# Performance work log

Hardware: AMD Instinct MI355X
Metric: run time of the kernel (lower is better)

Reference implementation:

```python
import jax, jax.numpy as jnp
import numpy as np


def _conv1d(x, w, b, pad):
    # x: (BN, Cin, L), w: (Cout, Cin, K) torch OIH layout
    y = jax.lax.conv_general_dilated(x, w, window_strides=(1,), padding=[(pad, pad)],
                                     dimension_numbers=('NCH', 'OIH', 'NCH'))
    return y + b[None, :, None]


def _mask_conv(m, k):
    # all-ones kernel conv then >=1 threshold (matches constant-init mask convs, no_grad)
    w = jnp.ones((1, 1, k), m.dtype)
    y = jax.lax.conv_general_dilated(m, w, window_strides=(1,), padding=[((k - 1) // 2, (k - 1) // 2)],
                                     dimension_numbers=('NCH', 'OIH', 'NCH'))
    return (y >= 1.0).astype(m.dtype)


def _branch(x, m, w1, b1, w2, b2, k):
    pad = (k - 1) // 2
    o = jax.nn.relu(_conv1d(x, w1, b1, pad))
    m = jax.lax.stop_gradient(_mask_conv(m, k))
    o = o * m
    o = jax.nn.relu(_conv1d(o, w2, b2, pad))
    m = jax.lax.stop_gradient(_mask_conv(m, k))
    return o * m


def _forward(all_xanes, all_xanes_mask, all_elem_info, all_elem_mask,
             w_b1c1, b_b1c1, w_b1c2, b_b1c2,
             w_b2c1, b_b2c1, w_b2c2, b_b2c2,
             w_b3c1, b_b3c1, w_b3c2, b_b3c2,
             w_xfc, b_xfc,
             w_float, b_float, atom_emb, type_emb,
             w_fuse, b_fuse,
             in_w, in_b, out_w, out_b,
             w_fc1, b_fc1, w_fc2, b_fc2):
    B, N, L = all_xanes.shape
    E, H = 64, 4
    dh = E // H
    # ---- MultiScaleXANESExtractor ----
    x = all_xanes.reshape(B * N, 1, L)
    m3 = jnp.broadcast_to(all_xanes_mask.reshape(B * N, 1, 1).astype(jnp.float32), (B * N, 1, L))
    o1 = _branch(x, m3, w_b1c1, b_b1c1, w_b1c2, b_b1c2, 3)
    o2 = _branch(x, m3, w_b2c1, b_b2c1, w_b2c2, b_b2c2, 5)
    o3 = _branch(x, m3, w_b3c1, b_b3c1, w_b3c2, b_b3c2, 7)
    cat = jnp.concatenate([o1, o2, o3], axis=1)  # (BN, 384, L)
    pooled = cat.reshape(B * N, 384, 10, L // 10).mean(-1).reshape(B * N, -1)  # AdaptiveAvgPool1d(10)
    xfeat = (pooled @ w_xfc.T + b_xfc).reshape(B, N, -1)  # (B, N, 32)
    valid = (m3.sum(axis=(1, 2)) > 0).astype(jnp.float32).reshape(B, N, 1)
    xfeat = xfeat * valid
    # ---- ElementsFeatureProcessor (vectorized gathers) ----
    maskf = all_elem_mask.astype(jnp.float32)
    masked = all_elem_info * maskf[..., None]
    ff = jax.nn.relu(masked[..., :5] @ w_float.T + b_float)  # (B, N, 16)
    an = masked[..., 5].astype(jnp.int32)
    et = masked[..., 6].astype(jnp.int32)
    valid_e = (maskf >= 0.5)
    inrange = (an >= 1) & (an <= 94)
    take = (valid_e & inrange).astype(jnp.float32)[..., None]
    ez = atom_emb[jnp.clip(an, 0, 94)] * take            # (B, N, 8)
    ety = type_emb[jnp.clip(et, 0, 5)] * take            # (B, N, 4)
    ff = ff * valid_e.astype(jnp.float32)[..., None]
    efeat = jnp.concatenate([ff, ez, ety], axis=-1) * maskf[..., None]  # (B, N, 28)
    # ---- FuseElementAndXANES ----
    fused = jnp.concatenate([xfeat, efeat], axis=-1) @ w_fuse.T + b_fuse
    fused = fused * maskf[..., None]  # (B, N, 64)
    # ---- AttentionAggregator (nn.MultiheadAttention, batch_first) ----
    qkv = fused @ in_w.T + in_b
    q, k, v = jnp.split(qkv, 3, axis=-1)
    q = q.reshape(B, N, H, dh)
    k = k.reshape(B, N, H, dh)
    v = v.reshape(B, N, H, dh)
    scores = jnp.einsum('bqhd,bkhd->bhqk', q, k) / jnp.sqrt(jnp.float32(dh))
    keymask = (maskf >= 0.5)
    scores = jnp.where(keymask[:, None, None, :], scores, jnp.float32(-1e30))
    attn = jax.nn.softmax(scores, axis=-1)
    ao = jnp.einsum('bhqk,bkhd->bqhd', attn, v).reshape(B, N, E)
    ao = ao @ out_w.T + out_b
    ao = ao * maskf[..., None]
    pooled2 = ao.sum(axis=1) / (maskf.sum(axis=1, keepdims=True) + 1e-8)
    h = jax.nn.relu(pooled2 @ w_fc1.T + b_fc1)
    return h @ w_fc2.T + b_fc2  # (B, num_classes)


def setup_inputs():
    key = jax.random.key(0)
    ks = jax.random.split(key, 40)
    B, N, L = 32, 16, 200
    all_xanes = jax.random.normal(ks[0], (B, N, L), jnp.float32)
    all_xanes_mask = jax.random.randint(ks[1], (B, N), 0, 2).astype(jnp.float32)
    ef = jax.random.normal(ks[2], (B, N, 7), jnp.float32)
    an = jax.random.randint(ks[3], (B, N), 1, 95).astype(jnp.float32)
    et = jax.random.randint(ks[4], (B, N), 0, 6).astype(jnp.float32)
    all_elem_info = ef.at[..., 5].set(an).at[..., 6].set(et)
    all_elem_mask = jax.random.randint(ks[5], (B, N), 0, 2).astype(jnp.float32)
    all_elem_mask = all_elem_mask.at[:, 0].set(1.0)  # avoid fully-padded rows (NaN softmax)

    def p(k, shape):
        return jax.random.normal(k, shape, jnp.float32) * 0.05

    inp = dict(all_xanes=all_xanes, all_xanes_mask=all_xanes_mask,
               all_elem_info=all_elem_info, all_elem_mask=all_elem_mask,
               w_b1c1=p(ks[6], (64, 1, 3)), b_b1c1=p(ks[7], (64,)),
               w_b1c2=p(ks[8], (128, 64, 3)), b_b1c2=p(ks[9], (128,)),
               w_b2c1=p(ks[10], (64, 1, 5)), b_b2c1=p(ks[11], (64,)),
               w_b2c2=p(ks[12], (128, 64, 5)), b_b2c2=p(ks[13], (128,)),
               w_b3c1=p(ks[14], (64, 1, 7)), b_b3c1=p(ks[15], (64,)),
               w_b3c2=p(ks[16], (128, 64, 7)), b_b3c2=p(ks[17], (128,)),
               w_xfc=p(ks[18], (32, 3840)), b_xfc=p(ks[19], (32,)),
               w_float=p(ks[20], (16, 5)), b_float=p(ks[21], (16,)),
               atom_emb=p(ks[22], (95, 8)), type_emb=p(ks[23], (6, 4)),
               w_fuse=p(ks[24], (64, 60)), b_fuse=p(ks[25], (64,)),
               in_w=p(ks[26], (192, 64)), in_b=p(ks[27], (192,)),
               out_w=p(ks[28], (64, 64)), out_b=p(ks[29], (64,)),
               w_fc1=p(ks[30], (64, 64)), b_fc1=p(ks[31], (64,)),
               w_fc2=p(ks[32], (1, 64)), b_fc2=p(ks[33], (1,)))
    return inp


def reference(all_xanes, all_xanes_mask, all_elem_info, all_elem_mask,
              w_b1c1, b_b1c1, w_b1c2, b_b1c2,
              w_b2c1, b_b2c1, w_b2c2, b_b2c2,
              w_b3c1, b_b3c1, w_b3c2, b_b3c2,
              w_xfc, b_xfc, w_float, b_float, atom_emb, type_emb,
              w_fuse, b_fuse, in_w, in_b, out_w, out_b,
              w_fc1, b_fc1, w_fc2, b_fc2):
    return _forward(all_xanes, all_xanes_mask, all_elem_info, all_elem_mask,
                    w_b1c1, b_b1c1, w_b1c2, b_b1c2,
                    w_b2c1, b_b2c1, w_b2c2, b_b2c2,
                    w_b3c1, b_b3c1, w_b3c2, b_b3c2,
                    w_xfc, b_xfc, w_float, b_float, atom_emb, type_emb,
                    w_fuse, b_fuse, in_w, in_b, out_w, out_b,
                    w_fc1, b_fc1, w_fc2, b_fc2)
```

## Files before the change

### kernel.cpp

```cpp
#include <hip/hip_runtime.h>
#include <math.h>

typedef float f32x4 __attribute__((ext_vector_type(4)));
typedef short short8 __attribute__((ext_vector_type(8)));

__device__ __forceinline__ short bf16r(float f) {
    union { float f; unsigned u; } x; x.f = f;
    unsigned u = x.u + 0x7fffu + ((x.u >> 16) & 1u);
    return (short)(u >> 16);
}

template<int K>
__device__ __forceinline__ void pack_branch(const float* __restrict__ w2,
                                            short* __restrict__ wpack, int u) {
    int lane = u & 63;
    int kb   = (u >> 6) & 1;
    int rem  = u >> 7;
    int j = rem % K, c = rem / K;
    int co  = c * 16 + (lane & 15);
    int cib = kb * 32 + 8 * ((lane >> 4) & 3);
    short8 v;
    #pragma unroll
    for (int i = 0; i < 8; ++i)
        v[i] = bf16r(w2[(co * 64 + (cib + i)) * K + j]);
    *reinterpret_cast<short8*>(wpack + (size_t)u * 8) = v;
}

__global__ __launch_bounds__(256) void pack_kernel(
    const float* __restrict__ w23, const float* __restrict__ w25,
    const float* __restrict__ w27,
    short* __restrict__ wp3, short* __restrict__ wp5, short* __restrict__ wp7)
{
    int tid = blockIdx.x * 256 + threadIdx.x;
    const int n3 = 8 * 3 * 2 * 64;
    const int n5 = 8 * 5 * 2 * 64;
    const int n7 = 8 * 7 * 2 * 64;
    if (tid < n3)                pack_branch<3>(w23, wp3, tid);
    else if (tid < n3 + n5)      pack_branch<5>(w25, wp5, tid - n3);
    else if (tid < n3 + n5 + n7) pack_branch<7>(w27, wp7, tid - n3 - n5);
}

template<int K, int LT0, int NLT>
__device__ __forceinline__ void mfma2c_pass(
    const short* t1s, const short* wpB0, const short* wpB1,
    int lane, f32x4* accA, f32x4* accB)
{
    constexpr int PAD = (K - 1) / 2;
    const int lane15 = lane & 15;
    const int g      = (lane >> 4) & 3;
    #pragma unroll
    for (int m = 0; m < 2 * K; ++m) {
        const int j = m >> 1, kb = m & 1;
        const short8 B0 = *reinterpret_cast<const short8*>(wpB0 + (size_t)m * 64 * 8);
        const short8 B1 = *reinterpret_cast<const short8*>(wpB1 + (size_t)m * 64 * 8);
        const int r   = LT0 * 16 + lane15 + 3 + j - PAD;
        const int col = (kb * 32 + 8 * g) ^ ((r & 7) << 3);
        const short* ab = &t1s[r * 64 + col];
        #pragma unroll
        for (int lt = 0; lt < NLT; ++lt) {
            const short8 af = *reinterpret_cast<const short8*>(ab + lt * 1024);
            accA[lt] = __builtin_amdgcn_mfma_f32_16x16x32_bf16(af, B0, accA[lt], 0, 0, 0);
            accB[lt] = __builtin_amdgcn_mfma_f32_16x16x32_bf16(af, B1, accB[lt], 0, 0, 0);
        }
    }
}

template<int GV, int LT0, int NLT>
__device__ __forceinline__ void pool_accum(const f32x4* acc, float bb, float* pb) {
    #pragma unroll
    for (int lt = 0; lt < NLT; ++lt) {
        #pragma unroll
        for (int r4 = 0; r4 < 4; ++r4) {
            const int l = (LT0 + lt) * 16 + 4 * GV + r4;
            if (l < 200)
                pb[l / 20] += fmaxf(acc[lt][r4] + bb, 0.0f);
        }
    }
}

template<int K, int LT0, int NLT>
__device__ __forceinline__ void do_pass(
    const short* t1s, const short* wpB0, const short* wpB1, int lane,
    float bb0, float bb1, float* pb0, float* pb1)
{
    const int g = (lane >> 4) & 3;
    f32x4 accA[NLT], accB[NLT];
    #pragma unroll
    for (int i = 0; i < NLT; ++i) {
        f32x4 z = {0.f, 0.f, 0.f, 0.f};
        accA[i] = z; accB[i] = z;
    }
    mfma2c_pass<K, LT0, NLT>(t1s, wpB0, wpB1, lane, accA, accB);
    if      (g == 0) { pool_accum<0, LT0, NLT>(accA, bb0, pb0); pool_accum<0, LT0, NLT>(accB, bb1, pb1); }
    else if (g == 1) { pool_accum<1, LT0, NLT>(accA, bb0, pb0); pool_accum<1, LT0, NLT>(accB, bb1, pb1); }
    else if (g == 2) { pool_accum<2, LT0, NLT>(accA, bb0, pb0); pool_accum<2, LT0, NLT>(accB, bb1, pb1); }
    else             { pool_accum<3, LT0, NLT>(accA, bb0, pb0); pool_accum<3, LT0, NLT>(accB, bb1, pb1); }
}

template<int K>
__device__ __forceinline__ void branch_body(
    const int bn, const int t,
    const float* __restrict__ x,
    const float* __restrict__ w1, const float* __restrict__ b1,
    const float* __restrict__ b2, const short* __restrict__ wpack,
    const float* __restrict__ w_xfc_br, float* __restrict__ xfeatP_br,
    float* xs, short* t1s, float* pooled_s, float* b2s)
{
    constexpr int PAD = (K - 1) / 2;
    const int lane = t & 63;
    const int w    = t >> 6;
    const int lane15 = lane & 15;

    if (t < 208) xs[t] = 0.0f;
    for (int idx = t; idx < 32 * 64; idx += 256) {
        int rr = idx >> 6;
        int row = (rr < 3) ? rr : (200 + rr);
        t1s[row * 64 + (idx & 63)] = 0;
    }
    if (t < 128) b2s[t] = b2[t];
    __syncthreads();

    if (t < 200) xs[3 + t] = x[bn * 200 + t];
    __syncthreads();

    {
        float w1_0 = w1[lane * K + 0], w1_1 = w1[lane * K + 1], w1_2 = w1[lane * K + 2];
        float w1_3 = 0.f, w1_4 = 0.f, w1_5 = 0.f, w1_6 = 0.f;
        if (K > 3) { w1_3 = w1[lane * K + 3]; w1_4 = w1[lane * K + 4]; }
        if (K > 5) { w1_5 = w1[lane * K + 5]; w1_6 = w1[lane * K + 6]; }
        const float b1r = b1[lane];
        for (int l = w; l < 200; l += 4) {
            const float* xp = &xs[3 + l - PAD];
            float a = b1r;
            a = fmaf(w1_0, xp[0], a);
            a = fmaf(w1_1, xp[1], a);
            a = fmaf(w1_2, xp[2], a);
            if (K > 3) { a = fmaf(w1_3, xp[3], a); a = fmaf(w1_4, xp[4], a); }
            if (K > 5) { a = fmaf(w1_5, xp[5], a); a = fmaf(w1_6, xp[6], a); }
            const int row = l + 3;
            t1s[row * 64 + (lane ^ ((row & 7) << 3))] = bf16r(fmaxf(a, 0.0f));
        }
    }
    __syncthreads();

    const int c0 = 2 * w, c1 = 2 * w + 1;
    const int coA = c0 * 16 + lane15, coB = c1 * 16 + lane15;
    const float bb0 = b2s[coA], bb1 = b2s[coB];
    const short* wpB0 = wpack + ((size_t)(c0 * 2 * K) * 64 + lane) * 8;
    const short* wpB1 = wpack + ((size_t)(c1 * 2 * K) * 64 + lane) * 8;

    float pb0[10], pb1[10];
    #pragma unroll
    for (int b = 0; b < 10; ++b) { pb0[b] = 0.0f; pb1[b] = 0.0f; }

    do_pass<K, 0, 5>(t1s, wpB0, wpB1, lane, bb0, bb1, pb0, pb1);
    do_pass<K, 5, 4>(t1s, wpB0, wpB1, lane, bb0, bb1, pb0, pb1);
    do_pass<K, 9, 4>(t1s, wpB0, wpB1, lane, bb0, bb1, pb0, pb1);

    #pragma unroll
    for (int b = 0; b < 10; ++b) {
        pb0[b] += __shfl_xor(pb0[b], 16);
        pb0[b] += __shfl_xor(pb0[b], 32);
        pb1[b] += __shfl_xor(pb1[b], 16);
        pb1[b] += __shfl_xor(pb1[b], 32);
    }
    if (lane < 16) {
        #pragma unroll
        for (int b = 0; b < 10; ++b) {
            pooled_s[coA * 10 + b] = pb0[b];
            pooled_s[coB * 10 + b] = pb1[b];
        }
    }
    __syncthreads();

    {
        const int o = t >> 3, part = t & 7;
        const f32x4* wr4 = reinterpret_cast<const f32x4*>(w_xfc_br + o * 3840);
        const f32x4* pp4 = reinterpret_cast<const f32x4*>(pooled_s);
        float s0 = 0.0f, s1 = 0.0f;
        #pragma unroll
        for (int i = 0; i < 40; ++i) {
            const f32x4 wv = wr4[part + 8 * i];
            const f32x4 pv = pp4[part + 8 * i];
            float s = wv[0] * pv[0];
            s = fmaf(wv[1], pv[1], s);
            s = fmaf(wv[2], pv[2], s);
            s = fmaf(wv[3], pv[3], s);
            if (i & 1) s1 += s; else s0 += s;
        }
        float a = s0 + s1;
        a += __shfl_xor(a, 1);
        a += __shfl_xor(a, 2);
        a += __shfl_xor(a, 4);
        if (part == 0) xfeatP_br[bn * 32 + o] = a * 0.05f;
    }
}

__global__ __launch_bounds__(256, 4) void branch_fused(
    const float* __restrict__ x, const float* __restrict__ xmask,
    const float* __restrict__ w1_3, const float* __restrict__ b1_3,
    const float* __restrict__ b2_3, const short* __restrict__ wp3,
    const float* __restrict__ w1_5, const float* __restrict__ b1_5,
    const float* __restrict__ b2_5, const short* __restrict__ wp5,
    const float* __restrict__ w1_7, const float* __restrict__ b1_7,
    const float* __restrict__ b2_7, const short* __restrict__ wp7,
    const float* __restrict__ w_xfc, float* __restrict__ xfeatP)
{
    __shared__ float xs[208];
    __shared__ short t1s[232 * 64];
    __shared__ __align__(16) float pooled_s[1280];
    __shared__ float b2s[128];

    const int bx = blockIdx.x;
    const int br = bx % 3;
    const int bn = bx / 3;
    const int t  = threadIdx.x;

    if (xmask[bn] == 0.0f) return;

    if (br == 0)
        branch_body<3>(bn, t, x, w1_3, b1_3, b2_3, wp3,
                       w_xfc,        xfeatP,             xs, t1s, pooled_s, b2s);
    else if (br == 1)
        branch_body<5>(bn, t, x, w1_5, b1_5, b2_5, wp5,
                       w_xfc + 1280, xfeatP + 512 * 32,  xs, t1s, pooled_s, b2s);
    else
        branch_body<7>(bn, t, x, w1_7, b1_7, b2_7, wp7,
                       w_xfc + 2560, xfeatP + 1024 * 32, xs, t1s, pooled_s, b2s);
}

__global__ __launch_bounds__(256) void tail_kernel(
    const float* __restrict__ xfeatP,
    const float* __restrict__ b_xfc,
    const float* __restrict__ xmaskp,
    const float* __restrict__ elem_info,
    const float* __restrict__ emaskp,
    const float* __restrict__ w_float, const float* __restrict__ b_float,
    const float* __restrict__ atom_emb, const float* __restrict__ type_emb,
    const float* __restrict__ w_fuse,  const float* __restrict__ b_fuse,
    const float* __restrict__ in_w,    const float* __restrict__ in_b,
    const float* __restrict__ out_w,   const float* __restrict__ out_b,
    const float* __restrict__ w_fc1,   const float* __restrict__ b_fc1,
    const float* __restrict__ w_fc2,   const float* __restrict__ b_fc2,
    float* __restrict__ out)
{
    const int b = blockIdx.x;
    const int t = threadIdx.x;

    __shared__ float fu[16][60];
    __shared__ float fused[16][64];
    __shared__ float qkvs[16][192];
    __shared__ float sc[4][16][16];
    __shared__ float ao[16][64];
    __shared__ float aoo[16][64];
    __shared__ float p2s[64];
    __shared__ float hs[64];
    __shared__ float em[16];

    if (t < 16) em[t] = emaskp[b * 16 + t];
    for (int d = t; d < 512; d += 256) {
        int n = d >> 5, o = d & 31;
        const int bn = b * 16 + n;
        float a = xfeatP[bn * 32 + o]
                + xfeatP[(512 + bn) * 32 + o]
                + xfeatP[(1024 + bn) * 32 + o];
        fu[n][o] = (a + b_xfc[o]) * xmaskp[bn];
    }
    __syncthreads();

    {
        int n = t >> 4, slot = t & 15;
        float m  = em[n];
        float vE = (m >= 0.5f) ? 1.0f : 0.0f;
        const float* ei = elem_info + (b * 16 + n) * 7;
        float a = b_float[slot];
        #pragma unroll
        for (int i = 0; i < 5; ++i)
            a = fmaf(ei[i] * m, w_float[slot * 5 + i], a);
        fu[n][32 + slot] = fmaxf(a, 0.0f) * vE * m;

        int an = (int)(ei[5] * m);
        int et = (int)(ei[6] * m);
        float take = (vE != 0.0f && an >= 1 && an <= 94) ? 1.0f : 0.0f;
        int anc = an < 0 ? 0 : (an > 94 ? 94 : an);
        int etc = et < 0 ? 0 : (et > 5 ? 5 : et);
        if (slot < 8)
            fu[n][48 + slot] = atom_emb[anc * 8 + slot] * take * m;
        else if (slot < 12)
            fu[n][56 + (slot - 8)] = type_emb[etc * 4 + (slot - 8)] * take * m;
    }
    __syncthreads();

    for (int d = t; d < 1024; d += 256) {
        int n = d >> 6, o = d & 63;
        float a = b_fuse[o];
        const float* wr = w_fuse + o * 60;
        #pragma unroll
        for (int i = 0; i < 60; ++i) a = fmaf(fu[n][i], wr[i], a);
        fused[n][o] = a * em[n];
    }
    __syncthreads();

    for (int d = t; d < 3072; d += 256) {
        int n = d / 192, rr = d - n * 192;
        float a = in_b[rr];
        const float* wr = in_w + rr * 64;
        #pragma unroll
        for (int i = 0; i < 64; ++i) a = fmaf(fused[n][i], wr[i], a);
        qkvs[n][rr] = a;
    }
    __syncthreads();

    for (int d = t; d < 1024; d += 256) {
        int h = d >> 8, i = (d >> 4) & 15, j = d & 15;
        float a = 0.0f;
        #pragma unroll
        for (int dd = 0; dd < 16; ++dd)
            a = fmaf(qkvs[i][h * 16 + dd], qkvs[j][64 + h * 16 + dd], a);
        a *= 0.25f;
        if (em[j] < 0.5f) a = -1e30f;
        sc[h][i][j] = a;
    }
    __syncthreads();

    if (t < 64) {
        int h = t >> 4, i = t & 15;
        float mx = -3.4e38f;
        #pragma unroll
        for (int j = 0; j < 16; ++j) mx = fmaxf(mx, sc[h][i][j]);
        float e[16];
        float s = 0.0f;
        #pragma unroll
        for (int j = 0; j < 16; ++j) { e[j] = expf(sc[h][i][j] - mx); s += e[j]; }
        float inv = 1.0f / s;
        #pragma unroll
        for (int j = 0; j < 16; ++j) sc[h][i][j] = e[j] * inv;
    }
    __syncthreads();

    for (int d = t; d < 1024; d += 256) {
        int n = d >> 6, e = d & 63, h = e >> 4;
        float a = 0.0f;
        #pragma unroll
        for (int j = 0; j < 16; ++j)
            a = fmaf(sc[h][n][j], qkvs[j][128 + e], a);
        ao[n][e] = a;
    }
    __syncthreads();

    for (int d = t; d < 1024; d += 256) {
        int n = d >> 6, o = d & 63;
        float a = out_b[o];
        const float* wr = out_w + o * 64;
        #pragma unroll
        for (int i = 0; i < 64; ++i) a = fmaf(ao[n][i], wr[i], a);
        aoo[n][o] = a * em[n];
    }
    __syncthreads();

    if (t < 64) {
        float s = 0.0f, ms = 0.0f;
        #pragma unroll
        for (int n = 0; n < 16; ++n) { s += aoo[n][t]; ms += em[n]; }
        p2s[t] = s / (ms + 1e-8f);
    }
    __syncthreads();

    if (t < 64) {
        float a = b_fc1[t];
        const float* wr = w_fc1 + t * 64;
        #pragma unroll
        for (int i = 0; i < 64; ++i) a = fmaf(p2s[i], wr[i], a);
        hs[t] = fmaxf(a, 0.0f);
    }
    __syncthreads();

    if (t < 64) {
        float v = hs[t] * w_fc2[t];
        #pragma unroll
        for (int d2 = 32; d2 >= 1; d2 >>= 1) v += __shfl_xor(v, d2);
        if (t == 0) out[b] = v + b_fc2[0];
    }
}

extern "C" void kernel_launch(void* const* d_in, const int* in_sizes, int n_in,
                              void* d_out, int out_size, void* d_ws, size_t ws_size,
                              hipStream_t stream)
{
    (void)in_sizes; (void)n_in; (void)out_size; (void)ws_size;
    const float* x     = (const float*)d_in[0];
    const float* xmask = (const float*)d_in[1];
    const float* einfo = (const float*)d_in[2];
    const float* emask = (const float*)d_in[3];

    float* xfeatP = (float*)d_ws;
    short* wp3 = (short*)(xfeatP + 3 * 512 * 32);
    short* wp5 = wp3 + 24576;
    short* wp7 = wp5 + 40960;

    pack_kernel<<<60, 256, 0, stream>>>(
        (const float*)d_in[6], (const float*)d_in[10], (const float*)d_in[14],
        wp3, wp5, wp7);

    branch_fused<<<1536, 256, 0, stream>>>(x, xmask,
        (const float*)d_in[4],  (const float*)d_in[5],  (const float*)d_in[7],  wp3,
        (const float*)d_in[8],  (const float*)d_in[9],  (const float*)d_in[11], wp5,
        (const float*)d_in[12], (const float*)d_in[13], (const float*)d_in[15], wp7,
        (const float*)d_in[16], xfeatP);

    tail_kernel<<<32, 256, 0, stream>>>(xfeatP,
        (const float*)d_in[17], xmask, einfo, emask,
        (const float*)d_in[18], (const float*)d_in[19],
        (const float*)d_in[20], (const float*)d_in[21],
        (const float*)d_in[22], (const float*)d_in[23],
        (const float*)d_in[24], (const float*)d_in[25],
        (const float*)d_in[26], (const float*)d_in[27],
        (const float*)d_in[28], (const float*)d_in[29],
        (const float*)d_in[30], (const float*)d_in[31],
        (float*)d_out);
}
```

Measured before the change: 86.81 us.

## Prefetch conv2 weights, widen MFMA passes, register-tile conv1 input window

The second-conv MFMA loop is no longer fully unrolled. It now software-pipelines the weight fragment loads, fetching the next tap's B operands while the current tap's MFMAs run. The L-tiling drops from three passes (5/4/4 tiles) to two (7/6), which raises accumulator register use in exchange for fewer weight reloads. The first conv now has each wave cover contiguous 25-row chunks, with the input window held in registers instead of re-read from LDS for every tap. Together these aim to cut global and LDS load latency and repeated loads, at the risk of more register pressure and lower occupancy.

```diff
diff --git a/kernel.cpp b/kernel.cpp
--- a/kernel.cpp
+++ b/kernel.cpp
@@ -41,26 +41,42 @@
 }
 
 template<int K, int LT0, int NLT>
-__device__ __forceinline__ void mfma2c_pass(
-    const short* t1s, const short* wpB0, const short* wpB1,
+__device__ __forceinline__ void mfma_pass2(
+    const short* __restrict__ t1s,
+    const short8* __restrict__ wpB0, const short8* __restrict__ wpB1,
     int lane, f32x4* accA, f32x4* accB)
 {
     constexpr int PAD = (K - 1) / 2;
     const int lane15 = lane & 15;
-    const int g      = (lane >> 4) & 3;
-    #pragma unroll
-    for (int m = 0; m < 2 * K; ++m) {
+    const int g8 = 8 * ((lane >> 4) & 3);
+    short8 bA = wpB0[0], bB = wpB1[0];
+    #pragma unroll 1
+    for (int m = 0; m < 2 * K - 1; ++m) {
+        const short8 nA = wpB0[(m + 1) * 64];
+        const short8 nB = wpB1[(m + 1) * 64];
         const int j = m >> 1, kb = m & 1;
-        const short8 B0 = *reinterpret_cast<const short8*>(wpB0 + (size_t)m * 64 * 8);
-        const short8 B1 = *reinterpret_cast<const short8*>(wpB1 + (size_t)m * 64 * 8);
-        const int r   = LT0 * 16 + lane15 + 3 + j - PAD;
-        const int col = (kb * 32 + 8 * g) ^ ((r & 7) << 3);
+        const int r = LT0 * 16 + lane15 + 3 + j - PAD;
+        const int col = (kb * 32 + g8) ^ ((r & 7) << 3);
         const short* ab = &t1s[r * 64 + col];
         #pragma unroll
         for (int lt = 0; lt < NLT; ++lt) {
             const short8 af = *reinterpret_cast<const short8*>(ab + lt * 1024);
-            accA[lt] = __builtin_amdgcn_mfma_f32_16x16x32_bf16(af, B0, accA[lt], 0, 0, 0);
-            accB[lt] = __builtin_amdgcn_mfma_f32_16x16x32_bf16(af, B1, accB[lt], 0, 0, 0);
+            accA[lt] = __builtin_amdgcn_mfma_f32_16x16x32_bf16(af, bA, accA[lt], 0, 0, 0);
+            accB[lt] = __builtin_amdgcn_mfma_f32_16x16x32_bf16(af, bB, accB[lt], 0, 0, 0);
+        }
+        bA = nA; bB = nB;
+    }
+    {
+        const int m = 2 * K - 1;
+        const int j = m >> 1, kb = m & 1;
+        const int r = LT0 * 16 + lane15 + 3 + j - PAD;
+        const int col = (kb * 32 + g8) ^ ((r & 7) << 3);
+        const short* ab = &t1s[r * 64 + col];
+        #pragma unroll
+        for (int lt = 0; lt < NLT; ++lt) {
+            const short8 af = *reinterpret_cast<const short8*>(ab + lt * 1024);
+            accA[lt] = __builtin_amdgcn_mfma_f32_16x16x32_bf16(af, bA, accA[lt], 0, 0, 0);
+            accB[lt] = __builtin_amdgcn_mfma_f32_16x16x32_bf16(af, bB, accB[lt], 0, 0, 0);
         }
     }
 }
@@ -79,9 +95,10 @@
 }
 
 template<int K, int LT0, int NLT>
-__device__ __forceinline__ void do_pass(
-    const short* t1s, const short* wpB0, const short* wpB1, int lane,
-    float bb0, float bb1, float* pb0, float* pb1)
+__device__ __forceinline__ void do_pass2(
+    const short* __restrict__ t1s,
+    const short8* __restrict__ wpB0, const short8* __restrict__ wpB1,
+    int lane, float bb0, float bb1, float* pb0, float* pb1)
 {
     const int g = (lane >> 4) & 3;
     f32x4 accA[NLT], accB[NLT];
@@ -90,7 +107,7 @@
         f32x4 z = {0.f, 0.f, 0.f, 0.f};
         accA[i] = z; accB[i] = z;
     }
-    mfma2c_pass<K, LT0, NLT>(t1s, wpB0, wpB1, lane, accA, accB);
+    mfma_pass2<K, LT0, NLT>(t1s, wpB0, wpB1, lane, accA, accB);
     if      (g == 0) { pool_accum<0, LT0, NLT>(accA, bb0, pb0); pool_accum<0, LT0, NLT>(accB, bb1, pb1); }
     else if (g == 1) { pool_accum<1, LT0, NLT>(accA, bb0, pb0); pool_accum<1, LT0, NLT>(accB, bb1, pb1); }
     else if (g == 2) { pool_accum<2, LT0, NLT>(accA, bb0, pb0); pool_accum<2, LT0, NLT>(accB, bb1, pb1); }
@@ -129,16 +146,29 @@
         if (K > 3) { w1_3 = w1[lane * K + 3]; w1_4 = w1[lane * K + 4]; }
         if (K > 5) { w1_5 = w1[lane * K + 5]; w1_6 = w1[lane * K + 6]; }
         const float b1r = b1[lane];
-        for (int l = w; l < 200; l += 4) {
-            const float* xp = &xs[3 + l - PAD];
-            float a = b1r;
-            a = fmaf(w1_0, xp[0], a);
-            a = fmaf(w1_1, xp[1], a);
-            a = fmaf(w1_2, xp[2], a);
-            if (K > 3) { a = fmaf(w1_3, xp[3], a); a = fmaf(w1_4, xp[4], a); }
-            if (K > 5) { a = fmaf(w1_5, xp[5], a); a = fmaf(w1_6, xp[6], a); }
-            const int row = l + 3;
-            t1s[row * 64 + (lane ^ ((row & 7) << 3))] = bf16r(fmaxf(a, 0.0f));
+        #pragma unroll 1
+        for (int ch = 0; ch < 2; ++ch) {
+            const int lb = 50 * w + 25 * ch;
+            float xr[31];
+            #pragma unroll
+            for (int i = 0; i < 31; ++i) xr[i] = xs[lb + i];
+            #pragma unroll
+            for (int ll = 0; ll < 25; ++ll) {
+                float a = b1r;
+                a = fmaf(w1_0, xr[ll + 3 - PAD + 0], a);
+                a = fmaf(w1_1, xr[ll + 3 - PAD + 1], a);
+                a = fmaf(w1_2, xr[ll + 3 - PAD + 2], a);
+                if (K > 3) {
+                    a = fmaf(w1_3, xr[ll + 3 - PAD + 3], a);
+                    a = fmaf(w1_4, xr[ll + 3 - PAD + 4], a);
+                }
+                if (K > 5) {
+                    a = fmaf(w1_5, xr[ll + 3 - PAD + 5], a);
+                    a = fmaf(w1_6, xr[ll + 3 - PAD + 6], a);
+                }
+                const int row = lb + ll + 3;
+                t1s[row * 64 + (lane ^ ((row & 7) << 3))] = bf16r(fmaxf(a, 0.0f));
+            }
         }
     }
     __syncthreads();
@@ -146,16 +176,17 @@
     const int c0 = 2 * w, c1 = 2 * w + 1;
     const int coA = c0 * 16 + lane15, coB = c1 * 16 + lane15;
     const float bb0 = b2s[coA], bb1 = b2s[coB];
-    const short* wpB0 = wpack + ((size_t)(c0 * 2 * K) * 64 + lane) * 8;
-    const short* wpB1 = wpack + ((size_t)(c1 * 2 * K) * 64 + lane) * 8;
+    const short8* wpB0 = reinterpret_cast<const short8*>(wpack)
+                         + (size_t)(c0 * 2 * K) * 64 + lane;
+    const short8* wpB1 = reinterpret_cast<const short8*>(wpack)
+                         + (size_t)(c1 * 2 * K) * 64 + lane;
 
     float pb0[10], pb1[10];
     #pragma unroll
     for (int b = 0; b < 10; ++b) { pb0[b] = 0.0f; pb1[b] = 0.0f; }
 
-    do_pass<K, 0, 5>(t1s, wpB0, wpB1, lane, bb0, bb1, pb0, pb1);
-    do_pass<K, 5, 4>(t1s, wpB0, wpB1, lane, bb0, bb1, pb0, pb1);
-    do_pass<K, 9, 4>(t1s, wpB0, wpB1, lane, bb0, bb1, pb0, pb1);
+    do_pass2<K, 0, 7>(t1s, wpB0, wpB1, lane, bb0, bb1, pb0, pb1);
+    do_pass2<K, 7, 6>(t1s, wpB0, wpB1, lane, bb0, bb1, pb0, pb1);
 
     #pragma unroll
     for (int b = 0; b < 10; ++b) {
```

Result: faster. 71.69 us (-17.4%).
